# Kernel tuning notes

Measured on AMD Instinct MI355X. Metric: run time of the kernel, lower is better.

The kernel has to match this reference:

```python
import jax, jax.numpy as jnp
import numpy as np

B, T, C = 8, 2048, 1024
N_HEAD = 16
HEAD_DIM = C // N_HEAD  # 64


def setup_inputs() -> dict:
    key = jax.random.key(0)
    k1, k2, k3 = jax.random.split(key, 3)
    x = jax.random.normal(k1, (B, T, C), dtype=jnp.float32)
    # qkv projection: Linear(C, 3*head_dim) with bias
    W = jax.random.normal(k2, (C, 3 * HEAD_DIM), dtype=jnp.float32) * (1.0 / np.sqrt(C))
    b = jax.random.normal(k3, (3 * HEAD_DIM,), dtype=jnp.float32) * 0.01
    return {"x": x, "W": W, "b": b}


def reference(x, W, b):
    # qkv projection, then chunk into (k, q, v) -- note key comes first in the original
    kqv = x @ W + b                       # [B, T, 3*hd]
    k, q, v = jnp.split(kqv, 3, axis=-1)  # each [B, T, hd]
    scale = HEAD_DIM ** -0.5
    wei = jnp.einsum('bth,bsh->bts', q, k) * scale  # [B, T, T]
    t = x.shape[1]
    causal = jnp.tril(jnp.ones((t, t), dtype=bool))
    wei = jnp.where(causal, wei, -jnp.inf)
    wei = jax.nn.softmax(wei, axis=-1)
    # dropout p=0.0 -> identity
    out = jnp.einsum('bts,bsh->bth', wei, v)  # [B, T, hd]
    return out
```

## Files before the change

### kernel.cpp

```cpp
#include <hip/hip_runtime.h>

#define NB 8
#define NT 2048
#define NC 1024
#define HD 64
#define N3 192

typedef float f32x4 __attribute__((ext_vector_type(4)));
typedef _Float16 f16x8 __attribute__((ext_vector_type(8)));
typedef short short8 __attribute__((ext_vector_type(8)));
typedef short short4v __attribute__((ext_vector_type(4)));

static __device__ __forceinline__ short f2h(float f) {
  _Float16 h = (_Float16)f;
  return __builtin_bit_cast(short, h);
}

typedef __attribute__((address_space(1))) const void* gptr1;
typedef __attribute__((address_space(3))) void* sptr3;
static __device__ __forceinline__ void gload_lds16(const void* g, void* s) {
  __builtin_amdgcn_global_load_lds((gptr1)g, (sptr3)s, 16, 0, 0);
}

__launch_bounds__(256)
__global__ void prep_w(const float* __restrict__ W, short* __restrict__ Wt) {
  const int n = threadIdx.x;
  if (n >= 192) return;
  const int k0 = blockIdx.x * 16;
  short8 v0, v1;
#pragma unroll
  for (int j = 0; j < 8; ++j) v0[j] = f2h(W[(size_t)(k0 + j) * N3 + n]);
#pragma unroll
  for (int j = 0; j < 8; ++j) v1[j] = f2h(W[(size_t)(k0 + 8 + j) * N3 + n]);
  *(short8*)(Wt + (size_t)n * NC + k0) = v0;
  *(short8*)(Wt + (size_t)n * NC + k0 + 8) = v1;
}

__launch_bounds__(256, 2)
__global__ void qkv_proj(const float* __restrict__ x, const short* __restrict__ Wt,
                         const float* __restrict__ bias, short* __restrict__ Kb,
                         short* __restrict__ Qb, short* __restrict__ Vt,
                         float* __restrict__ kmax2) {
  __shared__ short Ax[2][32 * 64];
  __shared__ short Bw[2][192 * 64];

  const int tid = threadIdx.x;
  const int lane = tid & 63;
  const int wave = tid >> 6;
  const int wr = wave >> 1, wc = wave & 1;
  const int r0 = blockIdx.x * 32;
  const int batch = r0 >> 11;
  const int t0 = r0 & (NT - 1);
  const int g = lane >> 4, c = lane & 15;

  const int bsub = lane >> 3;
  const size_t bgoff = (size_t)bsub * (NC * 2) + (size_t)((lane & 7) ^ bsub) * 16;

  f32x4 acc[6];
#pragma unroll
  for (int nt = 0; nt < 6; ++nt) acc[nt] = (f32x4){0.f, 0.f, 0.f, 0.f};

  float4 areg[2];

  auto stage_B = [&](int kt, int p) {
    const char* src = (const char*)Wt + (size_t)(wave * 48) * (NC * 2) +
                      (size_t)kt * 128 + bgoff;
    char* dst = (char*)Bw[p] + wave * 48 * 128;
#pragma unroll
    for (int j = 0; j < 6; ++j)
      gload_lds16(src + (size_t)(j * 8) * (NC * 2), dst + j * 8 * 128);
  };
  auto load_A = [&](int kt) {
    const float* xp = x + (size_t)r0 * NC + kt * 64;
#pragma unroll
    for (int i = 0; i < 2; ++i) {
      int idx = tid + 256 * i;
      int row = idx >> 4, c4 = idx & 15;
      areg[i] = *(const float4*)(xp + (size_t)row * NC + c4 * 4);
    }
  };
  auto write_A = [&](int p) {
#pragma unroll
    for (int i = 0; i < 2; ++i) {
      int idx = tid + 256 * i;
      int row = idx >> 4, c4 = idx & 15;
      int byte = row * 128 + ((c4 * 8) ^ ((row & 7) << 4));
      float4 v = areg[i];
      short4v h;
      h[0] = f2h(v.x); h[1] = f2h(v.y); h[2] = f2h(v.z); h[3] = f2h(v.w);
      *(short4v*)((char*)Ax[p] + byte) = h;
    }
  };
  auto compute = [&](int p) {
#pragma unroll
    for (int kc = 0; kc < 2; ++kc) {
      const int arow = wr * 16 + c;
      f16x8 a = *(const f16x8*)((const char*)Ax[p] + arow * 128 +
                                ((kc * 64 + (g << 4)) ^ ((arow & 7) << 4)));
#pragma unroll
      for (int nt = 0; nt < 6; ++nt) {
        const int brow = wc * 96 + nt * 16 + c;
        f16x8 b = *(const f16x8*)((const char*)Bw[p] + brow * 128 +
                                  ((kc * 64 + (g << 4)) ^ ((brow & 7) << 4)));
        acc[nt] = __builtin_amdgcn_mfma_f32_16x16x32_f16(a, b, acc[nt], 0, 0, 0);
      }
    }
  };

  stage_B(0, 0);
  load_A(0);
  write_A(0);
  __syncthreads();
#pragma unroll 1
  for (int kt = 0; kt < 16; ++kt) {
    const int p = kt & 1;
    if (kt < 15) { stage_B(kt + 1, p ^ 1); load_A(kt + 1); }
    compute(p);
    if (kt < 15) write_A(p ^ 1);
    __syncthreads();
  }

  float bv[6];
#pragma unroll
  for (int nt = 0; nt < 6; ++nt) bv[nt] = bias[wc * 96 + nt * 16 + c];

  short* VTl = (short*)Ax[0];
  float knorm[4] = {0.f, 0.f, 0.f, 0.f};
#pragma unroll
  for (int nt = 0; nt < 6; ++nt) {
#pragma unroll
    for (int i = 0; i < 4; ++i) {
      int n = wc * 96 + nt * 16 + c;
      int lrow = wr * 16 + (g << 2) + i;
      float v = acc[nt][i] + bv[nt];
      size_t tok = ((size_t)batch << 11) | (size_t)(t0 + lrow);
      if (n < 64) {
        Kb[tok * HD + n] = f2h(v);
        knorm[i] += v * v;
      } else if (n < 128) {
        Qb[tok * HD + (n - 64)] = f2h(v);
      } else {
        int h = n - 128;
        int byte = h * 64 + ((lrow * 2) ^ ((h & 3) << 4));
        *(short*)((char*)VTl + byte) = f2h(v);
      }
    }
  }
  if (wc == 0) {
#pragma unroll
    for (int d = 1; d < 16; d <<= 1)
#pragma unroll
      for (int i = 0; i < 4; ++i) knorm[i] += __shfl_xor(knorm[i], d);
    float mx = fmaxf(fmaxf(knorm[0], knorm[1]), fmaxf(knorm[2], knorm[3]));
    if (c == 0) atomicMax((int*)(kmax2 + batch), __float_as_int(mx));
  }
  __syncthreads();
  {
    int h = tid >> 2, ch = tid & 3;
    short8 v = *(const short8*)((const char*)VTl + h * 64 +
                                ((ch * 16) ^ ((h & 3) << 4)));
    *(short8*)(Vt + (((size_t)(batch * HD + h)) << 11) + (size_t)t0 + ch * 8) = v;
  }
}

__launch_bounds__(256)
__global__ void attn_part(const short* __restrict__ Kb, const short* __restrict__ Qb,
                          const short* __restrict__ Vt, const float* __restrict__ kmax2,
                          float* __restrict__ Opart, float* __restrict__ Lpart) {
  __shared__ short Kld[2][64 * 64];
  __shared__ short Vld[2][64 * 64];
  __shared__ short Pld[4][16 * 64];

  const int tid = threadIdx.x, lane = tid & 63, wave = tid >> 6;
  const int g = lane >> 4, c = lane & 15;
  const int bid = blockIdx.x;
  const int ch = bid & 3;
  const int qt = 31 - ((bid >> 2) & 31);
  const int b = bid >> 7;
  const int nkv = qt + 1;
  const int ks = ch * nkv / 4, ke = (ch + 1) * nkv / 4;
  if (ks == ke) return;
  const int q0 = qt * 64;
  const int slot = (b * 32 + qt) * 4 + ch;
  const float c2 = 0.125f * 1.44269504088896340736f;

  f16x8 qa[2];
  {
    size_t qbase = ((size_t)b * NT + (size_t)(q0 + wave * 16 + c)) * HD + (g << 3);
    qa[0] = *(const f16x8*)(Qb + qbase);
    qa[1] = *(const f16x8*)(Qb + qbase + 32);
  }
  float m2r[4];
  {
    const float kmaxn = sqrtf(kmax2[b]);
    float qn = 0.f;
#pragma unroll
    for (int kc = 0; kc < 2; ++kc)
#pragma unroll
      for (int j = 0; j < 8; ++j) {
        float qv = (float)qa[kc][j];
        qn += qv * qv;
      }
    qn += __shfl_xor(qn, 16);
    qn += __shfl_xor(qn, 32);
#pragma unroll
    for (int i = 0; i < 4; ++i)
      m2r[i] = sqrtf(__shfl(qn, (g << 2) + i)) * kmaxn * c2;
  }

  f32x4 o[5];
#pragma unroll
  for (int nt = 0; nt < 5; ++nt) o[nt] = (f32x4){0.f, 0.f, 0.f, 0.f};
  f16x8 bone;
#pragma unroll
  for (int j = 0; j < 8; ++j) bone[j] = (c == 0) ? (_Float16)1.0f : (_Float16)0.0f;

  const int sub = lane >> 3, chx = (lane & 7) ^ sub;
  const char* ksrc = (const char*)Kb + ((size_t)b * NT) * 128;
  const char* vsrc = (const char*)Vt + ((size_t)b * HD) * 4096;

  auto stage = [&](int t, int p) {
    const int s0 = t * 64;
    const char* kp = ksrc + (size_t)(s0 + wave * 16 + sub) * 128 + (size_t)chx * 16;
    const char* vp = vsrc + (size_t)(wave * 16 + sub) * 4096 + (size_t)s0 * 2 + (size_t)chx * 16;
    gload_lds16(kp, (char*)Kld[p] + (wave * 16) * 128);
    gload_lds16(kp + 8 * 128, (char*)Kld[p] + (wave * 16 + 8) * 128);
    gload_lds16(vp, (char*)Vld[p] + (wave * 16) * 128);
    gload_lds16(vp + (size_t)8 * 4096, (char*)Vld[p] + (wave * 16 + 8) * 128);
  };

  stage(ks, 0);
  __syncthreads();
  int p = 0;
#pragma unroll 1
  for (int t = ks; t < ke; ++t) {
    if (t + 1 < ke) stage(t + 1, p ^ 1);
    const int s0 = t * 64;

    f32x4 s[4];
#pragma unroll
    for (int st = 0; st < 4; ++st) s[st] = (f32x4){0.f, 0.f, 0.f, 0.f};
#pragma unroll
    for (int kc = 0; kc < 2; ++kc)
#pragma unroll
      for (int st = 0; st < 4; ++st) {
        int row = st * 16 + c;
        f16x8 bk = *(const f16x8*)((const char*)Kld[p] + row * 128 +
                                   ((kc * 64 + (g << 4)) ^ ((row & 7) << 4)));
        s[st] = __builtin_amdgcn_mfma_f32_16x16x32_f16(qa[kc], bk, s[st], 0, 0, 0);
      }

    const bool diag = (t == qt);
#pragma unroll
    for (int st = 0; st < 4; ++st)
#pragma unroll
      for (int i = 0; i < 4; ++i) {
        float pv = __builtin_amdgcn_exp2f(s[st][i] * c2 - m2r[i]);
        if (diag && (s0 + st * 16 + c) > (q0 + wave * 16 + (g << 2) + i)) pv = 0.f;
        int prow = (g << 2) + i;
        *(short*)((char*)Pld[wave] + prow * 128 +
                  (((st * 16 + c) * 2) ^ ((prow & 7) << 4))) = f2h(pv);
      }

#pragma unroll
    for (int kc = 0; kc < 2; ++kc) {
      f16x8 pa = *(const f16x8*)((const char*)Pld[wave] + c * 128 +
                                 ((kc * 64 + (g << 4)) ^ ((c & 7) << 4)));
#pragma unroll
      for (int nt = 0; nt < 4; ++nt) {
        int vrow = nt * 16 + c;
        f16x8 bv = *(const f16x8*)((const char*)Vld[p] + vrow * 128 +
                                   ((kc * 64 + (g << 4)) ^ ((vrow & 7) << 4)));
        o[nt] = __builtin_amdgcn_mfma_f32_16x16x32_f16(pa, bv, o[nt], 0, 0, 0);
      }
      o[4] = __builtin_amdgcn_mfma_f32_16x16x32_f16(pa, bone, o[4], 0, 0, 0);
    }
    __syncthreads();
    p ^= 1;
  }

  float* ob = Opart + (size_t)slot * 4096 + (size_t)(wave * 16) * 64;
#pragma unroll
  for (int i = 0; i < 4; ++i) {
    int r = (g << 2) + i;
#pragma unroll
    for (int nt = 0; nt < 4; ++nt) ob[r * 64 + nt * 16 + c] = o[nt][i];
  }
  if (c == 0) {
#pragma unroll
    for (int i = 0; i < 4; ++i)
      Lpart[slot * 64 + wave * 16 + (g << 2) + i] = o[4][i];
  }
}

__launch_bounds__(256)
__global__ void attn_comb(const float* __restrict__ Opart, const float* __restrict__ Lpart,
                          float* __restrict__ out) {
  const int qt = blockIdx.x & 31;
  const int b = blockIdx.x >> 5;
  const int nkv = qt + 1;
  const int t = threadIdx.x;
  const int base = (b * 32 + qt) * 4;

  f32x4 acc[4];
  float lsum[4];
#pragma unroll
  for (int j = 0; j < 4; ++j) { acc[j] = (f32x4){0.f, 0.f, 0.f, 0.f}; lsum[j] = 0.f; }

#pragma unroll
  for (int ch = 0; ch < 4; ++ch) {
    int ks = ch * nkv / 4, ke = (ch + 1) * nkv / 4;
    if (ks == ke) continue;
    const float* op = Opart + (size_t)(base + ch) * 4096;
    const float* lp = Lpart + (base + ch) * 64;
#pragma unroll
    for (int j = 0; j < 4; ++j) {
      int row = (t >> 4) + 16 * j;
      acc[j] += *(const f32x4*)(op + row * 64 + (t & 15) * 4);
      lsum[j] += lp[row];
    }
  }
  float* ob = out + ((size_t)b * NT + (size_t)qt * 64) * HD;
#pragma unroll
  for (int j = 0; j < 4; ++j) {
    int row = (t >> 4) + 16 * j;
    float inv = 1.0f / lsum[j];
    f32x4 v = acc[j];
    v[0] *= inv; v[1] *= inv; v[2] *= inv; v[3] *= inv;
    *(f32x4*)(ob + row * 64 + (t & 15) * 4) = v;
  }
}

extern "C" void kernel_launch(void* const* d_in, const int* in_sizes, int n_in,
                              void* d_out, int out_size, void* d_ws, size_t ws_size,
                              hipStream_t stream) {
  const float* x = (const float*)d_in[0];
  const float* W = (const float*)d_in[1];
  const float* bias = (const float*)d_in[2];
  float* out = (float*)d_out;

  char* ws = (char*)d_ws;
  float* kmax2 = (float*)ws;
  short* Wt = (short*)(ws + 256);
  short* Kb = Wt + (size_t)N3 * NC;
  short* Qb = Kb + (size_t)NB * NT * HD;
  short* Vt = Qb + (size_t)NB * NT * HD;
  float* Opart = (float*)(Vt + (size_t)NB * NT * HD);
  float* Lpart = Opart + (size_t)1024 * 4096;

  hipMemsetAsync(kmax2, 0, 8 * sizeof(float), stream);
  prep_w<<<64, 256, 0, stream>>>(W, Wt);
  qkv_proj<<<512, 256, 0, stream>>>(x, Wt, bias, Kb, Qb, Vt, kmax2);
  attn_part<<<NB * 32 * 4, 256, 0, stream>>>(Kb, Qb, Vt, kmax2, Opart, Lpart);
  attn_comb<<<NB * 32, 256, 0, stream>>>(Opart, Lpart, out);
}
```

Measured before the change: 141.8 us.

## Fuse attention combine into split-KV kernel and drop LDS staging of K/V

Folds the combine kernel into attn_part: the last chunk block for each query tile, chosen by an atomic counter, sums the partials and writes the output. It also removes the memset by zeroing kmax2 and the counters inside prep_w. The KV split becomes fixed 4-tile chunks over up to 8 blocks per query tile. K and V are now read straight from global memory into registers instead of being double-buffered through LDS, and the row sum is accumulated in registers rather than with an extra MFMA. These cut launch count and per-tile barriers, at the cost of uncoalesced direct global loads and a serial reduction tail in one block.

```diff
diff --git a/kernel.cpp b/kernel.cpp
--- a/kernel.cpp
+++ b/kernel.cpp
@@ -15,6 +15,11 @@
   _Float16 h = (_Float16)f;
   return __builtin_bit_cast(short, h);
 }
+static __device__ __forceinline__ unsigned pk2h(float a, float b) {
+  unsigned lo = (unsigned short)f2h(a);
+  unsigned hi = (unsigned short)f2h(b);
+  return lo | (hi << 16);
+}
 
 typedef __attribute__((address_space(1))) const void* gptr1;
 typedef __attribute__((address_space(3))) void* sptr3;
@@ -23,7 +28,12 @@
 }
 
 __launch_bounds__(256)
-__global__ void prep_w(const float* __restrict__ W, short* __restrict__ Wt) {
+__global__ void prep_w(const float* __restrict__ W, short* __restrict__ Wt,
+                       float* __restrict__ kmax2, int* __restrict__ cnt) {
+  if (blockIdx.x == 0) {
+    if (threadIdx.x < 256) cnt[threadIdx.x] = 0;
+    if (threadIdx.x < 8) kmax2[threadIdx.x] = 0.f;
+  }
   const int n = threadIdx.x;
   if (n >= 192) return;
   const int k0 = blockIdx.x * 16;
@@ -163,36 +173,38 @@
   }
 }
 
+#define PPITCH 136
 __launch_bounds__(256)
 __global__ void attn_part(const short* __restrict__ Kb, const short* __restrict__ Qb,
                           const short* __restrict__ Vt, const float* __restrict__ kmax2,
-                          float* __restrict__ Opart, float* __restrict__ Lpart) {
-  __shared__ short Kld[2][64 * 64];
-  __shared__ short Vld[2][64 * 64];
-  __shared__ short Pld[4][16 * 64];
+                          float* __restrict__ Opart, float* __restrict__ Lpart,
+                          int* __restrict__ cnt, float* __restrict__ out) {
+  __shared__ char Pl[4][16 * PPITCH];
+  __shared__ int flag;
 
   const int tid = threadIdx.x, lane = tid & 63, wave = tid >> 6;
   const int g = lane >> 4, c = lane & 15;
   const int bid = blockIdx.x;
-  const int ch = bid & 3;
-  const int qt = 31 - ((bid >> 2) & 31);
-  const int b = bid >> 7;
+  const int b = bid >> 8;
+  const int qtx = (bid >> 3) & 31;
+  const int ch = bid & 7;
+  const int qt = 31 - qtx;
   const int nkv = qt + 1;
-  const int ks = ch * nkv / 4, ke = (ch + 1) * nkv / 4;
-  if (ks == ke) return;
+  const int nch = (nkv + 3) >> 2;
+  if (ch >= nch) return;
+  const int ks = ch * 4, ke = min(ks + 4, nkv);
   const int q0 = qt * 64;
-  const int slot = (b * 32 + qt) * 4 + ch;
+  const int qg = q0 + wave * 16 + c;
   const float c2 = 0.125f * 1.44269504088896340736f;
 
   f16x8 qa[2];
   {
-    size_t qbase = ((size_t)b * NT + (size_t)(q0 + wave * 16 + c)) * HD + (g << 3);
-    qa[0] = *(const f16x8*)(Qb + qbase);
-    qa[1] = *(const f16x8*)(Qb + qbase + 32);
-  }
-  float m2r[4];
+    size_t base = ((size_t)b * NT + (size_t)qg) * HD + (g << 3);
+    qa[0] = *(const f16x8*)(Qb + base);
+    qa[1] = *(const f16x8*)(Qb + base + 32);
+  }
+  float m2;
   {
-    const float kmaxn = sqrtf(kmax2[b]);
     float qn = 0.f;
 #pragma unroll
     for (int kc = 0; kc < 2; ++kc)
@@ -203,82 +215,74 @@
       }
     qn += __shfl_xor(qn, 16);
     qn += __shfl_xor(qn, 32);
-#pragma unroll
-    for (int i = 0; i < 4; ++i)
-      m2r[i] = sqrtf(__shfl(qn, (g << 2) + i)) * kmaxn * c2;
-  }
-
-  f32x4 o[5];
-#pragma unroll
-  for (int nt = 0; nt < 5; ++nt) o[nt] = (f32x4){0.f, 0.f, 0.f, 0.f};
-  f16x8 bone;
-#pragma unroll
-  for (int j = 0; j < 8; ++j) bone[j] = (c == 0) ? (_Float16)1.0f : (_Float16)0.0f;
-
-  const int sub = lane >> 3, chx = (lane & 7) ^ sub;
-  const char* ksrc = (const char*)Kb + ((size_t)b * NT) * 128;
-  const char* vsrc = (const char*)Vt + ((size_t)b * HD) * 4096;
-
-  auto stage = [&](int t, int p) {
-    const int s0 = t * 64;
-    const char* kp = ksrc + (size_t)(s0 + wave * 16 + sub) * 128 + (size_t)chx * 16;
-    const char* vp = vsrc + (size_t)(wave * 16 + sub) * 4096 + (size_t)s0 * 2 + (size_t)chx * 16;
-    gload_lds16(kp, (char*)Kld[p] + (wave * 16) * 128);
-    gload_lds16(kp + 8 * 128, (char*)Kld[p] + (wave * 16 + 8) * 128);
-    gload_lds16(vp, (char*)Vld[p] + (wave * 16) * 128);
-    gload_lds16(vp + (size_t)8 * 4096, (char*)Vld[p] + (wave * 16 + 8) * 128);
-  };
-
-  stage(ks, 0);
-  __syncthreads();
-  int p = 0;
+    m2 = sqrtf(qn) * sqrtf(kmax2[b]) * c2;
+  }
+
+  f32x4 o[4];
+#pragma unroll
+  for (int nt = 0; nt < 4; ++nt) o[nt] = (f32x4){0.f, 0.f, 0.f, 0.f};
+  float l_r = 0.f;
+
+  const short* kbp = Kb + ((size_t)b * NT) * HD;
+  const short* vbp = Vt + (((size_t)b * HD) << 11);
+  char* pw = Pl[wave];
+
 #pragma unroll 1
   for (int t = ks; t < ke; ++t) {
-    if (t + 1 < ke) stage(t + 1, p ^ 1);
     const int s0 = t * 64;
-
+    f16x8 kfr[4][2];
+#pragma unroll
+    for (int st = 0; st < 4; ++st) {
+      size_t rb = (size_t)(s0 + st * 16 + c) * HD + (g << 3);
+      kfr[st][0] = *(const f16x8*)(kbp + rb);
+      kfr[st][1] = *(const f16x8*)(kbp + rb + 32);
+    }
     f32x4 s[4];
 #pragma unroll
     for (int st = 0; st < 4; ++st) s[st] = (f32x4){0.f, 0.f, 0.f, 0.f};
 #pragma unroll
     for (int kc = 0; kc < 2; ++kc)
 #pragma unroll
-      for (int st = 0; st < 4; ++st) {
-        int row = st * 16 + c;
-        f16x8 bk = *(const f16x8*)((const char*)Kld[p] + row * 128 +
-                                   ((kc * 64 + (g << 4)) ^ ((row & 7) << 4)));
-        s[st] = __builtin_amdgcn_mfma_f32_16x16x32_f16(qa[kc], bk, s[st], 0, 0, 0);
-      }
+      for (int st = 0; st < 4; ++st)
+        s[st] = __builtin_amdgcn_mfma_f32_16x16x32_f16(kfr[st][kc], qa[kc], s[st], 0, 0, 0);
 
     const bool diag = (t == qt);
 #pragma unroll
-    for (int st = 0; st < 4; ++st)
+    for (int st = 0; st < 4; ++st) {
+      float pv[4];
 #pragma unroll
       for (int i = 0; i < 4; ++i) {
-        float pv = __builtin_amdgcn_exp2f(s[st][i] * c2 - m2r[i]);
-        if (diag && (s0 + st * 16 + c) > (q0 + wave * 16 + (g << 2) + i)) pv = 0.f;
-        int prow = (g << 2) + i;
-        *(short*)((char*)Pld[wave] + prow * 128 +
-                  (((st * 16 + c) * 2) ^ ((prow & 7) << 4))) = f2h(pv);
-      }
+        int sg = s0 + st * 16 + (g << 2) + i;
+        float p = __builtin_amdgcn_exp2f(s[st][i] * c2 - m2);
+        pv[i] = (diag && sg > qg) ? 0.f : p;
+      }
+      l_r += (pv[0] + pv[1]) + (pv[2] + pv[3]);
+      uint2 w;
+      w.x = pk2h(pv[0], pv[1]);
+      w.y = pk2h(pv[2], pv[3]);
+      *(uint2*)(pw + c * PPITCH + st * 32 + g * 8) = w;
+    }
 
 #pragma unroll
     for (int kc = 0; kc < 2; ++kc) {
-      f16x8 pa = *(const f16x8*)((const char*)Pld[wave] + c * 128 +
-                                 ((kc * 64 + (g << 4)) ^ ((c & 7) << 4)));
+      uint2 h0 = *(const uint2*)(pw + c * PPITCH + kc * 64 + g * 16);
+      uint2 h1 = *(const uint2*)(pw + c * PPITCH + kc * 64 + g * 16 + 8);
+      f16x8 pa;
+      *(uint2*)&pa = h0;
+      *((uint2*)&pa + 1) = h1;
 #pragma unroll
       for (int nt = 0; nt < 4; ++nt) {
-        int vrow = nt * 16 + c;
-        f16x8 bv = *(const f16x8*)((const char*)Vld[p] + vrow * 128 +
-                                   ((kc * 64 + (g << 4)) ^ ((vrow & 7) << 4)));
-        o[nt] = __builtin_amdgcn_mfma_f32_16x16x32_f16(pa, bv, o[nt], 0, 0, 0);
-      }
-      o[4] = __builtin_amdgcn_mfma_f32_16x16x32_f16(pa, bone, o[4], 0, 0, 0);
-    }
-    __syncthreads();
-    p ^= 1;
-  }
-
+        f16x8 vv = *(const f16x8*)(vbp + (((size_t)(nt * 16 + c)) << 11) +
+                                   s0 + kc * 32 + (g << 3));
+        o[nt] = __builtin_amdgcn_mfma_f32_16x16x32_f16(pa, vv, o[nt], 0, 0, 0);
+      }
+    }
+  }
+
+  l_r += __shfl_xor(l_r, 16);
+  l_r += __shfl_xor(l_r, 32);
+
+  const int slot = ((b * 32 + qt) << 3) + ch;
   float* ob = Opart + (size_t)slot * 4096 + (size_t)(wave * 16) * 64;
 #pragma unroll
   for (int i = 0; i < 4; ++i) {
@@ -286,48 +290,42 @@
 #pragma unroll
     for (int nt = 0; nt < 4; ++nt) ob[r * 64 + nt * 16 + c] = o[nt][i];
   }
-  if (c == 0) {
-#pragma unroll
-    for (int i = 0; i < 4; ++i)
-      Lpart[slot * 64 + wave * 16 + (g << 2) + i] = o[4][i];
-  }
-}
-
-__launch_bounds__(256)
-__global__ void attn_comb(const float* __restrict__ Opart, const float* __restrict__ Lpart,
-                          float* __restrict__ out) {
-  const int qt = blockIdx.x & 31;
-  const int b = blockIdx.x >> 5;
-  const int nkv = qt + 1;
-  const int t = threadIdx.x;
-  const int base = (b * 32 + qt) * 4;
-
+  if (g == 0) Lpart[slot * 64 + wave * 16 + c] = l_r;
+
+  __syncthreads();
+  if (tid == 0) {
+    __threadfence();
+    int old = atomicAdd(&cnt[b * 32 + qt], 1);
+    flag = (old == nch - 1) ? 1 : 0;
+  }
+  __syncthreads();
+  if (!flag) return;
+  __threadfence();
+
+  const int base = (b * 32 + qt) << 3;
   f32x4 acc[4];
-  float lsum[4];
-#pragma unroll
-  for (int j = 0; j < 4; ++j) { acc[j] = (f32x4){0.f, 0.f, 0.f, 0.f}; lsum[j] = 0.f; }
-
-#pragma unroll
-  for (int ch = 0; ch < 4; ++ch) {
-    int ks = ch * nkv / 4, ke = (ch + 1) * nkv / 4;
-    if (ks == ke) continue;
-    const float* op = Opart + (size_t)(base + ch) * 4096;
-    const float* lp = Lpart + (base + ch) * 64;
+  float ls[4];
+#pragma unroll
+  for (int j = 0; j < 4; ++j) { acc[j] = (f32x4){0.f, 0.f, 0.f, 0.f}; ls[j] = 0.f; }
+#pragma unroll 1
+  for (int c2i = 0; c2i < nch; ++c2i) {
+    const float* op = Opart + (size_t)(base + c2i) * 4096;
+    const float* lp = Lpart + (base + c2i) * 64;
 #pragma unroll
     for (int j = 0; j < 4; ++j) {
-      int row = (t >> 4) + 16 * j;
-      acc[j] += *(const f32x4*)(op + row * 64 + (t & 15) * 4);
-      lsum[j] += lp[row];
-    }
-  }
-  float* ob = out + ((size_t)b * NT + (size_t)qt * 64) * HD;
+      int row = (tid >> 4) + 16 * j;
+      acc[j] += *(const f32x4*)(op + row * 64 + (tid & 15) * 4);
+      ls[j] += lp[row];
+    }
+  }
+  float* outb = out + ((size_t)b * NT + (size_t)q0) * HD;
 #pragma unroll
   for (int j = 0; j < 4; ++j) {
-    int row = (t >> 4) + 16 * j;
-    float inv = 1.0f / lsum[j];
+    int row = (tid >> 4) + 16 * j;
+    float inv = 1.0f / ls[j];
     f32x4 v = acc[j];
     v[0] *= inv; v[1] *= inv; v[2] *= inv; v[3] *= inv;
-    *(f32x4*)(ob + row * 64 + (t & 15) * 4) = v;
+    *(f32x4*)(outb + row * 64 + (tid & 15) * 4) = v;
   }
 }
 
@@ -341,16 +339,15 @@
 
   char* ws = (char*)d_ws;
   float* kmax2 = (float*)ws;
-  short* Wt = (short*)(ws + 256);
+  int* cnt = (int*)(ws + 256);
+  short* Wt = (short*)(ws + 2048);
   short* Kb = Wt + (size_t)N3 * NC;
   short* Qb = Kb + (size_t)NB * NT * HD;
   short* Vt = Qb + (size_t)NB * NT * HD;
   float* Opart = (float*)(Vt + (size_t)NB * NT * HD);
-  float* Lpart = Opart + (size_t)1024 * 4096;
-
-  hipMemsetAsync(kmax2, 0, 8 * sizeof(float), stream);
-  prep_w<<<64, 256, 0, stream>>>(W, Wt);
+  float* Lpart = Opart + (size_t)2048 * 4096;
+
+  prep_w<<<64, 256, 0, stream>>>(W, Wt, kmax2, cnt);
   qkv_proj<<<512, 256, 0, stream>>>(x, Wt, bias, Kb, Qb, Vt, kmax2);
-  attn_part<<<NB * 32 * 4, 256, 0, stream>>>(Kb, Qb, Vt, kmax2, Opart, Lpart);
-  attn_comb<<<NB * 32, 256, 0, stream>>>(Opart, Lpart, out);
-}
+  attn_part<<<NB * 32 * 8, 256, 0, stream>>>(Kb, Qb, Vt, kmax2, Opart, Lpart, cnt, out);
+}
```

After: 440.2 us. 210% more time.
